# Kernel optimization log

Measured on AMD Instinct MI355X. Metric: run time of the kernel, lower is better.

The kernel has to match this reference:

```python
import jax, jax.numpy as jnp
import numpy as np

K = 64
PI = np.float32(np.pi)


def setup_inputs() -> dict:
    key = jax.random.key(0)
    k1, k2 = jax.random.split(key)
    B, N = 4096, 21
    rotation = jax.random.normal(k1, (B, N, 3, 3), dtype=jnp.float32)
    conditions = jax.random.normal(k2, (B, N, 4 * K), dtype=jnp.float32)
    permute = np.arange(3).astype(np.int64)  # static permutation indices
    return {"rotation": rotation, "conditions": conditions, "permute": permute}


def _mobius_forward(rotation, conditions, p0, p1, p2):
    B, N = rotation.shape[0], rotation.shape[1]
    I3 = jnp.eye(3, dtype=rotation.dtype)

    x = rotation[..., p0]  # [B,N,3]
    y = rotation[..., p1]  # [B,N,3]

    # compute_mcl_parameters_nd
    weights = conditions[..., :K]                      # [B,N,K]
    w = conditions[..., K:].reshape(B, N, K, 3)        # [B,N,K,3]
    proj = I3 - jnp.einsum('bni,bnj->bnij', y, y)      # [B,N,3,3]
    w = jnp.einsum('bnij,bnkj->bnki', proj, w)
    r = -x
    r = r / jnp.linalg.norm(r, axis=-1, keepdims=True)
    v = jnp.cross(y, r)
    v = v / jnp.linalg.norm(v, axis=-1, keepdims=True)
    weights = jax.nn.softplus(weights)
    weights = weights / jnp.sum(weights, axis=-1, keepdims=True)
    w_norm = jnp.linalg.norm(w, axis=-1, keepdims=True)
    w = 0.7 / (1.0 + w_norm) * w

    # _forward_nd
    z = x
    zw = z[:, :, None, :] - w                          # [B,N,K,3]
    zw_norm = jnp.linalg.norm(zw, axis=-1)             # [B,N,K]
    w_norm2 = jnp.sum(w * w, axis=-1)                  # [B,N,K]
    h_z = ((1.0 - w_norm2) / zw_norm ** 2)[..., None] * zw - w  # [B,N,K,3]

    radians = jnp.arctan2(jnp.einsum('bnki,bni->bnk', h_z, v),
                          jnp.einsum('bnki,bni->bnk', h_z, r))
    ang = jnp.where(radians >= 0, radians, radians + 2.0 * PI)
    ang = jnp.sum(weights * ang, axis=2, keepdims=True)          # [B,N,1]
    tx = r * jnp.cos(ang) + v * jnp.sin(ang)                     # [B,N,3]

    zw_unit = zw / zw_norm[..., None]
    theta = jnp.arctan2(jnp.einsum('bni,bni->bn', x, v),
                        jnp.einsum('bni,bni->bn', x, r))[..., None]  # [B,N,1]
    dz_dtheta = -jnp.sin(theta) * r + jnp.cos(theta) * v             # [B,N,3]
    dh_dz = (1.0 - w_norm2)[..., None, None] * (
        I3 - 2.0 * jnp.einsum('bnki,bnkj->bnkij', zw_unit, zw_unit)
    ) / (zw_norm ** 2)[..., None, None]                              # [B,N,K,3,3]
    dh_dtheta = jnp.einsum('bnkpq,bnq->bnkp', dh_dz, dz_dtheta)      # [B,N,K,3]
    dtx = jnp.sum(jnp.linalg.norm(dh_dtheta, axis=-1) * weights, axis=2)  # [B,N]
    ldj = jnp.log(dtx)

    if (p1 - p0 == 1) or (p1 - p0 == -2):
        tz = jnp.cross(tx, y)
    else:
        tz = jnp.cross(y, tx)
    tz = tz / jnp.linalg.norm(tz, axis=-1, keepdims=True)

    cols = [None, None, None]
    cols[p0] = tx
    cols[p1] = y
    cols[p2] = tz
    trotation = jnp.stack(cols, axis=-1)  # [B,N,3,3]
    return trotation, jnp.sum(ldj, axis=-1)


def reference(rotation, conditions, permute):
    p0, p1, p2 = int(permute[0]), int(permute[1]), int(permute[2])
    return _mobius_forward(rotation, conditions, p0, p1, p2)
```

## Files before the change

kernel.cpp:

```cpp
#include <hip/hip_runtime.h>
#include <math.h>

#define PI_F    3.14159265358979323846f
#define TWO_PI  6.28318530717958647692f
#define HALF_PI 1.57079632679489661923f

__device__ __forceinline__ float frcp(float x)  { return __builtin_amdgcn_rcpf(x); }
__device__ __forceinline__ float frsq(float x)  { return __builtin_amdgcn_rsqf(x); }
__device__ __forceinline__ float fsqrt(float x) { return __builtin_amdgcn_sqrtf(x); }

__device__ __forceinline__ float fast_atan2_2pi(float y, float x) {
    float ax = fabsf(x), ay = fabsf(y);
    float mx = fmaxf(ax, ay), mn = fminf(ax, ay);
    float a  = (mx > 0.0f) ? mn * frcp(mx) : 0.0f;
    float s  = a * a;
    float r  = fmaf(s, fmaf(s, fmaf(s, fmaf(s, 0.0208351f, -0.085133f),
                                    0.180141f), -0.3302995f), 0.9998660f) * a;
    if (ay > ax) r = HALF_PI - r;
    if (x < 0.0f) r = PI_F - r;
    return (y < 0.0f) ? (TWO_PI - r) : r;
}

__global__ __launch_bounds__(448)
void mobius_fwd(const float* __restrict__ rot,
                const float* __restrict__ cond,
                const void* __restrict__ perm,
                float* __restrict__ out,
                int B, int N)
{
    const int wave = threadIdx.x >> 6;
    const int lane = threadIdx.x & 63;
    const int sub  = lane >> 4;
    const int j    = lane & 15;
    const int nwav = blockDim.x >> 6;

    const int b0     = blockIdx.x * 4;
    const int nb     = min(4, B - b0);
    const int nit    = N * nb;
    const int nquads = (nit + 3) >> 2;

    const int* pi = (const int*)perm;
    int p0 = pi[0], p1 = pi[1], p2 = pi[2];
    bool pok = ((unsigned)p0 < 3u) && ((unsigned)p1 < 3u) && ((unsigned)p2 < 3u)
               && (p0 != p1) && (p0 != p2) && (p1 != p2);
    if (!pok) {
        const long long* pl = (const long long*)perm;
        p0 = (int)pl[0]; p1 = (int)pl[1]; p2 = (int)pl[2];
    }
    const int dd = p1 - p0;
    const bool swapc = (dd == 1 || dd == -2);

    __shared__ __align__(16) float smem[7][4][264];
    __shared__ float s_ldj[256];

    const size_t base_item = (size_t)b0 * N;

    for (int q = wave; q < nquads; q += nwav) {
        float4 stg0, stg1, stg2, stg3;
        {
            int s0i = min(4 * q + 0, nit - 1);
            int s1i = min(4 * q + 1, nit - 1);
            int s2i = min(4 * q + 2, nit - 1);
            int s3i = min(4 * q + 3, nit - 1);
            stg0 = ((const float4*)(cond + (base_item + s0i) * 256))[lane];
            stg1 = ((const float4*)(cond + (base_item + s1i) * 256))[lane];
            stg2 = ((const float4*)(cond + (base_item + s2i) * 256))[lane];
            stg3 = ((const float4*)(cond + (base_item + s3i) * 256))[lane];
        }

        const int  i0    = 4 * q + sub;
        const bool valid = (i0 < nit);
        const int  iv    = valid ? i0 : 0;
        const size_t item = base_item + iv;

        const float* R = rot + item * 9;
        float x0 = R[p0], x1 = R[3 + p0], x2 = R[6 + p0];
        float y0 = R[p1], y1 = R[3 + p1], y2 = R[6 + p1];

        float xn2    = x0 * x0 + x1 * x1 + x2 * x2;
        float inv_xn = frsq(xn2);
        float xn     = xn2 * inv_xn;
        float xy     = x0 * y0 + x1 * y1 + x2 * y2;
        float yn2    = y0 * y0 + y1 * y1 + y2 * y2;
        float negA   = yn2 - 2.0f;

        float cv0 = x1 * y2 - x2 * y1;
        float cv1 = x2 * y0 - x0 * y2;
        float cv2 = x0 * y1 - x1 * y0;
        float inv_cn = frsq(cv0 * cv0 + cv1 * cv1 + cv2 * cv2);
        float v0 = cv0 * inv_cn, v1 = cv1 * inv_cn, v2 = cv2 * inv_cn;

        *(float4*)&smem[wave][0][4 * lane] = stg0;
        *(float4*)&smem[wave][1][4 * lane] = stg1;
        *(float4*)&smem[wave][2][4 * lane] = stg2;
        *(float4*)&smem[wave][3][4 * lane] = stg3;

        const float* myl = &smem[wave][sub][0];
        float4 pw4 = *(const float4*)(myl + 4 * j);
        float4 fa  = *(const float4*)(myl + 64 + 12 * j);
        float4 fb  = *(const float4*)(myl + 68 + 12 * j);
        float4 fc  = *(const float4*)(myl + 72 + 12 * j);

        float PW[4] = {pw4.x, pw4.y, pw4.z, pw4.w};
        float W0[4] = {fa.x, fa.w, fb.z, fc.y};
        float W1[4] = {fa.y, fb.x, fb.w, fc.z};
        float W2[4] = {fa.z, fb.y, fc.x, fc.w};

        float pp = 0.0f, pa = 0.0f, pd = 0.0f;
        #pragma unroll
        for (int cc = 0; cc < 4; ++cc) {
            float w0 = W0[cc], w1 = W1[cc], w2 = W2[cc];
            float yw  = y0 * w0 + y1 * w1 + y2 * w2;
            float wp2 = w0 * w0 + w1 * w1 + w2 * w2;
            float xwp = x0 * w0 + x1 * w1 + x2 * w2;
            float vwp = v0 * w0 + v1 * w1 + v2 * w2;
            float qn  = fmaxf(fmaf(yw * yw, negA, wp2), 0.0f);
            float sc  = 0.7f * frcp(1.0f + fsqrt(qn));
            float wn2 = (sc * sc) * qn;
            float xw  = sc * fmaf(-xy, yw, xwp);
            float zwn2 = fmaf(-2.0f, xw, xn2 + wn2);
            float c   = (1.0f - wn2) * frcp(zwn2);
            float cp1 = c + 1.0f;
            float hv  = -(cp1 * (sc * vwp));
            float hr  = fmaf(cp1, xw * inv_xn, -(c * xn));
            float ang = fast_atan2_2pi(hv, hr);
            float p   = __logf(1.0f + __expf(PW[cc]));
            pp += p; pa = fmaf(p, ang, pa); pd = fmaf(p, c, pd);
        }

        #pragma unroll
        for (int off = 8; off >= 1; off >>= 1) {
            pp += __shfl_xor(pp, off, 64);
            pa += __shfl_xor(pa, off, 64);
            pd += __shfl_xor(pd, off, 64);
        }

        float ip   = frcp(pp);
        float angT = pa * ip;
        float ldj  = __logf(pd * ip);

        float sa, ca;
        __sincosf(angT, &sa, &ca);
        float r0 = -x0 * inv_xn, r1 = -x1 * inv_xn, r2 = -x2 * inv_xn;
        float t0 = fmaf(r0, ca, v0 * sa);
        float t1 = fmaf(r1, ca, v1 * sa);
        float t2 = fmaf(r2, ca, v2 * sa);

        float u0, u1, u2;
        if (swapc) {
            u0 = t1 * y2 - t2 * y1;
            u1 = t2 * y0 - t0 * y2;
            u2 = t0 * y1 - t1 * y0;
        } else {
            u0 = y1 * t2 - y2 * t1;
            u1 = y2 * t0 - y0 * t2;
            u2 = y0 * t1 - y1 * t0;
        }
        float iun = frsq(u0 * u0 + u1 * u1 + u2 * u2);
        u0 *= iun; u1 *= iun; u2 *= iun;

        if (valid) {
            if (j < 9) {
                int row = (j >= 6) ? 2 : (j >= 3) ? 1 : 0;
                int cp  = j - 3 * row;
                float tr = (row == 0) ? t0 : (row == 1) ? t1 : t2;
                float yr = (row == 0) ? y0 : (row == 1) ? y1 : y2;
                float ur = (row == 0) ? u0 : (row == 1) ? u1 : u2;
                float val = (cp == p0) ? tr : (cp == p1) ? yr : ur;
                out[item * 9 + j] = val;
            }
            if (j == 0) s_ldj[i0] = ldj;
        }
    }

    __syncthreads();
    if (threadIdx.x < nb) {
        float acc = 0.0f;
        for (int n = 0; n < N; ++n) acc += s_ldj[threadIdx.x * N + n];
        out[(size_t)B * N * 9 + b0 + threadIdx.x] = acc;
    }
}

extern "C" void kernel_launch(void* const* d_in, const int* in_sizes, int n_in,
                              void* d_out, int out_size, void* d_ws, size_t ws_size,
                              hipStream_t stream) {
    const float* rot  = (const float*)d_in[0];
    const float* cond = (const float*)d_in[1];
    const void*  perm = d_in[2];
    float* out = (float*)d_out;

    int items = in_sizes[0] / 9;
    int B = out_size - items * 9;
    int N = items / B;

    int grid = (B + 3) / 4;
    mobius_fwd<<<dim3(grid), dim3(448), 0, stream>>>(rot, cond, perm, out, B, N);
}
```

Measured before the change: 26.55 us.

## Load conditions directly into registers and prefetch next quad

Removes the LDS staging buffer: each lane now reads its own slice of the conditions row and the rotation columns straight from global memory instead of doing coalesced float4 loads and redistributing them through shared memory. A software-pipelined register double buffer loads the next quad's data while the current quad is computed. This drops the LDS writes and reads, but the direct per-lane loads use a strided pattern (12-float stride), which may coalesce less well, and the extra live registers may lower occupancy.

```diff
diff --git a/kernel.cpp b/kernel.cpp
--- a/kernel.cpp
+++ b/kernel.cpp
@@ -20,6 +20,11 @@
     if (x < 0.0f) r = PI_F - r;
     return (y < 0.0f) ? (TWO_PI - r) : r;
 }
+
+struct QD {
+    float4 pw4, fa, fb, fc;
+    float x0, x1, x2, y0, y1, y2;
+};
 
 __global__ __launch_bounds__(448)
 void mobius_fwd(const float* __restrict__ rot,
@@ -50,32 +55,35 @@
     const int dd = p1 - p0;
     const bool swapc = (dd == 1 || dd == -2);
 
-    __shared__ __align__(16) float smem[7][4][264];
-    __shared__ float s_ldj[256];
+    __shared__ float s_ldj[128];
 
     const size_t base_item = (size_t)b0 * N;
 
+    auto loadq = [&](QD& d, int q) {
+        int iv = min(4 * q + sub, nit - 1);
+        const float* C = cond + (base_item + iv) * 256;
+        d.pw4 = *(const float4*)(C + 4 * j);
+        d.fa  = *(const float4*)(C + 64 + 12 * j);
+        d.fb  = *(const float4*)(C + 68 + 12 * j);
+        d.fc  = *(const float4*)(C + 72 + 12 * j);
+        const float* R = rot + (base_item + iv) * 9;
+        d.x0 = R[p0]; d.x1 = R[3 + p0]; d.x2 = R[6 + p0];
+        d.y0 = R[p1]; d.y1 = R[3 + p1]; d.y2 = R[6 + p1];
+    };
+
+    QD cur{}, nxt{};
+    if (wave < nquads) loadq(cur, wave);
+
     for (int q = wave; q < nquads; q += nwav) {
-        float4 stg0, stg1, stg2, stg3;
-        {
-            int s0i = min(4 * q + 0, nit - 1);
-            int s1i = min(4 * q + 1, nit - 1);
-            int s2i = min(4 * q + 2, nit - 1);
-            int s3i = min(4 * q + 3, nit - 1);
-            stg0 = ((const float4*)(cond + (base_item + s0i) * 256))[lane];
-            stg1 = ((const float4*)(cond + (base_item + s1i) * 256))[lane];
-            stg2 = ((const float4*)(cond + (base_item + s2i) * 256))[lane];
-            stg3 = ((const float4*)(cond + (base_item + s3i) * 256))[lane];
-        }
+        const int q2 = q + nwav;
+        if (q2 < nquads) loadq(nxt, q2);
 
         const int  i0    = 4 * q + sub;
         const bool valid = (i0 < nit);
-        const int  iv    = valid ? i0 : 0;
-        const size_t item = base_item + iv;
+        const size_t item = base_item + min(i0, nit - 1);
 
-        const float* R = rot + item * 9;
-        float x0 = R[p0], x1 = R[3 + p0], x2 = R[6 + p0];
-        float y0 = R[p1], y1 = R[3 + p1], y2 = R[6 + p1];
+        const float x0 = cur.x0, x1 = cur.x1, x2 = cur.x2;
+        const float y0 = cur.y0, y1 = cur.y1, y2 = cur.y2;
 
         float xn2    = x0 * x0 + x1 * x1 + x2 * x2;
         float inv_xn = frsq(xn2);
@@ -90,21 +98,10 @@
         float inv_cn = frsq(cv0 * cv0 + cv1 * cv1 + cv2 * cv2);
         float v0 = cv0 * inv_cn, v1 = cv1 * inv_cn, v2 = cv2 * inv_cn;
 
-        *(float4*)&smem[wave][0][4 * lane] = stg0;
-        *(float4*)&smem[wave][1][4 * lane] = stg1;
-        *(float4*)&smem[wave][2][4 * lane] = stg2;
-        *(float4*)&smem[wave][3][4 * lane] = stg3;
-
-        const float* myl = &smem[wave][sub][0];
-        float4 pw4 = *(const float4*)(myl + 4 * j);
-        float4 fa  = *(const float4*)(myl + 64 + 12 * j);
-        float4 fb  = *(const float4*)(myl + 68 + 12 * j);
-        float4 fc  = *(const float4*)(myl + 72 + 12 * j);
-
-        float PW[4] = {pw4.x, pw4.y, pw4.z, pw4.w};
-        float W0[4] = {fa.x, fa.w, fb.z, fc.y};
-        float W1[4] = {fa.y, fb.x, fb.w, fc.z};
-        float W2[4] = {fa.z, fb.y, fc.x, fc.w};
+        float PW[4] = {cur.pw4.x, cur.pw4.y, cur.pw4.z, cur.pw4.w};
+        float W0[4] = {cur.fa.x, cur.fa.w, cur.fb.z, cur.fc.y};
+        float W1[4] = {cur.fa.y, cur.fb.x, cur.fb.w, cur.fc.z};
+        float W2[4] = {cur.fa.z, cur.fb.y, cur.fc.x, cur.fc.w};
 
         float pp = 0.0f, pa = 0.0f, pd = 0.0f;
         #pragma unroll
@@ -171,6 +168,8 @@
             }
             if (j == 0) s_ldj[i0] = ldj;
         }
+
+        cur = nxt;
     }
 
     __syncthreads();
```

Measured after the change: 29.82 us. 12.3% more time.
